# Performance work log

Measured on AMD Instinct MI355X. Metric: run time of the kernel, lower is better.

Reference implementation:

```python
import jax, jax.numpy as jnp
from jax import lax
import numpy as np

NEG_INF = -1000000000.0  # matches torch masked_fill value
POS_THRESH = -100000000.0


def setup_inputs() -> dict:
    key = jax.random.key(0)
    k1, k2, k3 = jax.random.split(key, 3)
    B, C_in, L = 1, 16, 2048
    C_out, groups, K = 16, 4, 3
    scores = jax.random.normal(k1, (B, C_in, L, L), dtype=jnp.float32)
    weight = jax.random.normal(k2, (C_out, C_in // groups, K, K), dtype=jnp.float32) * 0.1
    bias = jax.random.normal(k3, (C_out,), dtype=jnp.float32) * 0.1
    return {"scores": scores, "weight": weight, "bias": bias}


def reference(scores, weight, bias):
    B, C_in, L, _ = scores.shape
    C_out, cpg, K, _ = weight.shape
    groups = C_in // cpg
    mask = jnp.tril(jnp.ones((L, L), dtype=bool))[None, None]  # (1,1,L,L) causal

    s = scores.astype(jnp.float32)
    z = jnp.where(mask, s, NEG_INF)

    # sparsemax over last axis: sort desc, cumsum, support-size threshold
    z_sorted = -jnp.sort(-z, axis=-1)                 # descending
    cum_sum = jnp.cumsum(z_sorted, axis=-1)
    k_idx = jnp.arange(1, L + 1, dtype=z.dtype)        # (L,) broadcasts over (B,C,L,L)
    cond = (1.0 + k_idx * z_sorted > cum_sum) & (z_sorted > POS_THRESH)
    k_sp = jnp.sum(cond, axis=-1, keepdims=True)       # support size, int
    k_safe = jnp.maximum(k_sp, 1)
    cum_sum_k = jnp.take_along_axis(cum_sum, k_safe - 1, axis=-1)
    tau = (cum_sum_k - 1.0) / k_safe.astype(z.dtype)
    tau = jnp.where(k_sp == 0, jnp.inf, tau)
    probs = jnp.maximum(z - tau, 0.0)                  # (B,C_in,L,L)

    # grouped same-padded conv2d over the (L,L) score map
    out = lax.conv_general_dilated(
        probs, weight,
        window_strides=(1, 1),
        padding=[(K // 2, K // 2), (K // 2, K // 2)],
        feature_group_count=groups,
        dimension_numbers=("NCHW", "OIHW", "NCHW"),
    )
    out = out + bias[None, :, None, None]
    out = jnp.where(mask, out, 0.0)
    return out.astype(scores.dtype)
```

## Files before the change

### kernel.cpp

```cpp
#include <hip/hip_runtime.h>

#define L 2048
#define CIN 16
#define GROUPS 4
#define NEG_INF  -1000000000.0f
#define POS_THRESH -100000000.0f

__global__ __launch_bounds__(256) void tau_kernel(const float* __restrict__ scores,
                                                  float* __restrict__ tau_out) {
    const int wid  = (blockIdx.x << 2) + (threadIdx.x >> 6);
    const int lane = threadIdx.x & 63;
    const int ws   = threadIdx.x >> 6;
    const int ch   = wid >> 11;
    const int row  = wid & 2047;
    const int n    = row + 1;
    const float* zrow = scores + ((size_t)ch * L + row) * L;

    float v[32];
    float m = NEG_INF;
#pragma unroll
    for (int j = 0; j < 8; ++j) {
        int c4 = lane + (j << 6);
        int c  = c4 << 2;
        float4 z = make_float4(NEG_INF, NEG_INF, NEG_INF, NEG_INF);
        if (c < n) z = *((const float4*)zrow + c4);
        v[4*j+0] = (c + 0 < n) ? z.x : NEG_INF;
        v[4*j+1] = (c + 1 < n) ? z.y : NEG_INF;
        v[4*j+2] = (c + 2 < n) ? z.z : NEG_INF;
        v[4*j+3] = (c + 3 < n) ? z.w : NEG_INF;
        m = fmaxf(m, fmaxf(fmaxf(v[4*j+0], v[4*j+1]), fmaxf(v[4*j+2], v[4*j+3])));
    }
#pragma unroll
    for (int d = 32; d; d >>= 1) m = fmaxf(m, __shfl_xor(m, d, 64));

    const float thr = m - 1.0f;

    __shared__ float buf[4][64];
    int base = 0;
#pragma unroll
    for (int j = 0; j < 32; ++j) {
        bool p = v[j] > thr;
        unsigned long long mask = __ballot(p);
        if (mask) {
            if (p) {
                int pos = __builtin_amdgcn_mbcnt_lo((unsigned)mask, 0);
                pos = __builtin_amdgcn_mbcnt_hi((unsigned)(mask >> 32), pos);
                pos += base;
                if (pos < 64) buf[ws][pos] = v[j];
            }
            base += __popcll(mask);
        }
    }
    __syncthreads();
    const int cnt = base;

    float tau;
    if (cnt <= 64) {
        float x = (lane < cnt) ? buf[ws][lane] : NEG_INF;
#pragma unroll
        for (int k = 2; k <= 64; k <<= 1) {
#pragma unroll
            for (int j = k >> 1; j > 0; j >>= 1) {
                float p = __shfl_xor(x, j, 64);
                bool desc    = ((lane & k) == 0);
                bool earlier = ((lane & j) == 0);
                float mx = fmaxf(x, p), mn = fminf(x, p);
                x = (desc == earlier) ? mx : mn;
            }
        }
        float csum = x;
#pragma unroll
        for (int d = 1; d < 64; d <<= 1) {
            float y = __shfl_up(csum, d, 64);
            if (lane >= d) csum += y;
        }
        bool cond = (1.0f + (float)(lane + 1) * x > csum) && (x > POS_THRESH);
        unsigned long long cmask = __ballot(cond);
        int k = (int)__popcll(cmask);
        float ck = __shfl(csum, k - 1, 64);
        tau = (ck - 1.0f) / (float)k;
    } else {
        tau = thr;
        int k_prev = -1;
        for (int it = 0; it < 64; ++it) {
            float S = 0.0f, Kf = 0.0f;
#pragma unroll
            for (int j = 0; j < 32; ++j)
                if (v[j] > tau) { S += v[j]; Kf += 1.0f; }
#pragma unroll
            for (int d = 32; d; d >>= 1) {
                S  += __shfl_xor(S,  d, 64);
                Kf += __shfl_xor(Kf, d, 64);
            }
            int K = (int)Kf;
            if (K == k_prev) break;
            tau = (S - 1.0f) / Kf;
            k_prev = K;
        }
    }
    if (lane == 0) tau_out[ch * L + row] = tau;
}

#define TR 16
#define TC 64
#define HR 18
#define PST 68

struct W6 { float l, m0, m1, m2, m3, r; };

__device__ __forceinline__ float rfl(float x) {
    return __builtin_bit_cast(float,
        __builtin_amdgcn_readfirstlane(__builtin_bit_cast(int, x)));
}

__global__ __launch_bounds__(256, 4) void conv_kernel(const float* __restrict__ scores,
                                                      const float* __restrict__ tau,
                                                      const float* __restrict__ weight,
                                                      const float* __restrict__ bias,
                                                      float* __restrict__ out) {
    const int c0 = blockIdx.x * TC;
    const int r0 = blockIdx.y * TR;
    const int g  = blockIdx.z;
    const int t  = threadIdx.x;

    if (c0 > r0 + TR - 1) {
        const float4 z4 = make_float4(0.f, 0.f, 0.f, 0.f);
#pragma unroll
        for (int jj = 0; jj < 4; ++jj) {
            int idx = t + (jj << 8);
            int c4  = idx & 15;
            int r   = (idx >> 4) & 15;
            int o   = idx >> 8;
            float4* p = (float4*)(out + (((size_t)((g << 2) + o) * L + (r0 + r)) * L + c0)) + c4;
            *p = z4;
        }
        return;
    }

    __shared__ __align__(16) float P[4][HR][PST];

    const bool interior = (c0 >= 1) && (c0 + TC + 1 <= r0) && (r0 + TR <= L - 1);

    const float* sbase = scores + (size_t)(g << 2) * L * L;
    const float* tbase = tau + (g << 2) * L;

    float4 zr[5];
    float  tvr[5];

    if (interior) {
#pragma unroll
        for (int jj = 0; jj < 5; ++jj) {
            int idx = t + (jj << 8);
            if (idx < 1152) {
                int hr = idx >> 6, ic = (idx >> 4) & 3, c4 = idx & 15;
                int r  = r0 - 1 + hr;
                zr[jj]  = *((const float4*)(sbase + (size_t)ic * L * L + (size_t)r * L + c0) + c4);
                tvr[jj] = tbase[ic * L + r];
            }
        }
        float hv = 0.f;
        int hic = 0, hhr = 0, hside = 0;
        if (t < 144) {
            hside = t & 1;
            int j = t >> 1;
            hic = j / HR; hhr = j - hic * HR;
            int r = r0 - 1 + hhr;
            int c = hside ? (c0 + TC) : (c0 - 1);
            hv = fmaxf(sbase[(size_t)hic * L * L + (size_t)r * L + c] - tbase[hic * L + r], 0.f);
        }
#pragma unroll
        for (int jj = 0; jj < 5; ++jj) {
            int idx = t + (jj << 8);
            if (idx < 1152) {
                int hr = idx >> 6, ic = (idx >> 4) & 3, c4 = idx & 15;
                float tv = tvr[jj];
                float4 z = zr[jj];
                float4 val;
                val.x = fmaxf(z.x - tv, 0.f);
                val.y = fmaxf(z.y - tv, 0.f);
                val.z = fmaxf(z.z - tv, 0.f);
                val.w = fmaxf(z.w - tv, 0.f);
                *((float4*)&P[ic][hr][c4 << 2]) = val;
            }
        }
        if (t < 144) P[hic][hhr][hside ? TC : 67] = hv;
    } else {
#pragma unroll
        for (int jj = 0; jj < 5; ++jj) {
            int idx = t + (jj << 8);
            zr[jj] = make_float4(0.f, 0.f, 0.f, 0.f);
            tvr[jj] = 0.f;
            if (idx < 1152) {
                int hr = idx >> 6, ic = (idx >> 4) & 3, c4 = idx & 15;
                int r  = r0 - 1 + hr;
                int cb = c0 + (c4 << 2);
                if (r >= 0 && r < L && cb <= r) {
                    zr[jj]  = *((const float4*)(sbase + (size_t)ic * L * L + (size_t)r * L) + (cb >> 2));
                    tvr[jj] = tbase[ic * L + r];
                }
            }
        }
        float hv = 0.f;
        int hic = 0, hhr = 0, hside = 0;
        if (t < 144) {
            hside = t & 1;
            int j = t >> 1;
            hic = j / HR; hhr = j - hic * HR;
            int r = r0 - 1 + hhr;
            int c = hside ? (c0 + TC) : (c0 - 1);
            if (r >= 0 && r < L && c >= 0 && c <= r)
                hv = fmaxf(sbase[(size_t)hic * L * L + (size_t)r * L + c] - tbase[hic * L + r], 0.f);
        }
#pragma unroll
        for (int jj = 0; jj < 5; ++jj) {
            int idx = t + (jj << 8);
            if (idx < 1152) {
                int hr = idx >> 6, ic = (idx >> 4) & 3, c4 = idx & 15;
                int r  = r0 - 1 + hr;
                int cb = c0 + (c4 << 2);
                float tv = tvr[jj];
                float4 z = zr[jj];
                float4 val = make_float4(0.f, 0.f, 0.f, 0.f);
                if (r >= 0 && r < L && cb <= r) {
                    val.x = fmaxf(z.x - tv, 0.f);
                    val.y = (cb + 1 <= r) ? fmaxf(z.y - tv, 0.f) : 0.f;
                    val.z = (cb + 2 <= r) ? fmaxf(z.z - tv, 0.f) : 0.f;
                    val.w = (cb + 3 <= r) ? fmaxf(z.w - tv, 0.f) : 0.f;
                }
                *((float4*)&P[ic][hr][c4 << 2]) = val;
            }
        }
        if (t < 144) P[hic][hhr][hside ? TC : 67] = hv;
    }
    __syncthreads();

    const int w4   = t >> 6;
    const int lane = t & 63;
    const int col4 = lane & 15;
    const int rloc = lane >> 4;
    const int ro   = (w4 << 2) + rloc;
    const int obase = g << 2;
    const int cb   = c0 + (col4 << 2);
    const int li   = col4 ? ((col4 << 2) - 2) : 66;
    const int ri   = (col4 << 2) + 4;

    auto ldwin = [&](int ic, int hr) -> W6 {
        const float* rp = &P[ic][hr][0];
        float4 M  = *(const float4*)(rp + (col4 << 2));
        float2 Lv = *(const float2*)(rp + li);
        float2 Rv = *(const float2*)(rp + ri);
        W6 q; q.l = Lv.y; q.m0 = M.x; q.m1 = M.y; q.m2 = M.z; q.m3 = M.w; q.r = Rv.x;
        return q;
    };

    float4 acc[4];
#pragma unroll
    for (int oc = 0; oc < 4; ++oc) {
        float bb = rfl(bias[obase + oc]);
        acc[oc] = make_float4(bb, bb, bb, bb);
    }

#define ROWFMA(q, wa, wb, wc, A)                                           \
    A.x = fmaf(q.l,  wa, fmaf(q.m0, wb, fmaf(q.m1, wc, A.x)));             \
    A.y = fmaf(q.m0, wa, fmaf(q.m1, wb, fmaf(q.m2, wc, A.y)));             \
    A.z = fmaf(q.m1, wa, fmaf(q.m2, wb, fmaf(q.m3, wc, A.z)));             \
    A.w = fmaf(q.m2, wa, fmaf(q.m3, wb, fmaf(q.r,  wc, A.w)));

#pragma unroll
    for (int ic = 0; ic < 4; ++ic) {
        W6 q0 = ldwin(ic, ro);
        W6 q1 = ldwin(ic, ro + 1);
        W6 q2 = ldwin(ic, ro + 2);
#pragma unroll
        for (int oc = 0; oc < 4; ++oc) {
            const float* wp = weight + (((obase + oc) << 2) + ic) * 9;
            const float w00 = rfl(wp[0]), w01 = rfl(wp[1]), w02 = rfl(wp[2]);
            const float w10 = rfl(wp[3]), w11 = rfl(wp[4]), w12 = rfl(wp[5]);
            const float w20 = rfl(wp[6]), w21 = rfl(wp[7]), w22 = rfl(wp[8]);
            ROWFMA(q0, w00, w01, w02, acc[oc])
            ROWFMA(q1, w10, w11, w12, acc[oc])
            ROWFMA(q2, w20, w21, w22, acc[oc])
        }
    }
#undef ROWFMA

    const int r_out = r0 + ro;
    if (interior) {
#pragma unroll
        for (int oc = 0; oc < 4; ++oc) {
            float* outp = out + ((size_t)(obase + oc) * L + r_out) * L + cb;
            *(float4*)outp = acc[oc];
        }
    } else {
#pragma unroll
        for (int oc = 0; oc < 4; ++oc) {
            float4 res;
            res.x = (cb     <= r_out) ? acc[oc].x : 0.f;
            res.y = (cb + 1 <= r_out) ? acc[oc].y : 0.f;
            res.z = (cb + 2 <= r_out) ? acc[oc].z : 0.f;
            res.w = (cb + 3 <= r_out) ? acc[oc].w : 0.f;
            float* outp = out + ((size_t)(obase + oc) * L + r_out) * L + cb;
            *(float4*)outp = res;
        }
    }
}

extern "C" void kernel_launch(void* const* d_in, const int* in_sizes, int n_in,
                              void* d_out, int out_size, void* d_ws, size_t ws_size,
                              hipStream_t stream) {
    const float* scores = (const float*)d_in[0];
    const float* weight = (const float*)d_in[1];
    const float* bias   = (const float*)d_in[2];
    float* out = (float*)d_out;
    float* tau = (float*)d_ws;

    tau_kernel<<<(CIN * L) / 4, 256, 0, stream>>>(scores, tau);

    dim3 gridB(L / TC, L / TR, GROUPS);
    conv_kernel<<<gridB, 256, 0, stream>>>(scores, tau, weight, bias, out);
}
```

Baseline: 486.0 us.

## Double-buffer per-input-channel probability tiles in conv kernel shared memory

Instead of loading all four input channels' sparsemax-probability tiles into shared memory before computing, the conv kernel now stages one channel at a time in a two-slot shared buffer. It prefetches the next channel into registers while computing the current one. This halves shared memory per block, which may allow more blocks per CU, and overlaps global loads with FMA work. The cost is an extra barrier per channel and a longer serial dependency chain inside each block. The edge path now fills masked lanes with tau so they evaluate to zero.

```diff
diff --git a/kernel.cpp b/kernel.cpp
--- a/kernel.cpp
+++ b/kernel.cpp
@@ -107,10 +107,84 @@
 #define PST 68
 
 struct W6 { float l, m0, m1, m2, m3, r; };
+struct Stage { float4 z0, z1; float tv0, tv1, hv; };
 
 __device__ __forceinline__ float rfl(float x) {
     return __builtin_bit_cast(float,
         __builtin_amdgcn_readfirstlane(__builtin_bit_cast(int, x)));
+}
+
+template<bool CHK>
+__device__ __forceinline__ void load_stage(Stage& s, const float* __restrict__ sb,
+                                           const float* __restrict__ tb,
+                                           int r0, int c0, int t) {
+    const int hr = t >> 4, c4 = t & 15;
+    const int r  = r0 - 1 + hr;
+    const int cb = c0 + (c4 << 2);
+    if (!CHK) {
+        s.z0  = *((const float4*)(sb + (size_t)r * L + c0) + c4);
+        s.tv0 = tb[r];
+    } else {
+        s.z0 = make_float4(0.f, 0.f, 0.f, 0.f); s.tv0 = 0.f;
+        if (r >= 0 && r < L && cb <= r) {
+            s.z0  = *((const float4*)(sb + (size_t)r * L) + (cb >> 2));
+            s.tv0 = tb[r];
+            if (cb + 1 > r) s.z0.y = s.tv0;
+            if (cb + 2 > r) s.z0.z = s.tv0;
+            if (cb + 3 > r) s.z0.w = s.tv0;
+        }
+    }
+    if (t < 32) {
+        const int r1 = r0 + 15 + (t >> 4);
+        if (!CHK) {
+            s.z1  = *((const float4*)(sb + (size_t)r1 * L + c0) + c4);
+            s.tv1 = tb[r1];
+        } else {
+            s.z1 = make_float4(0.f, 0.f, 0.f, 0.f); s.tv1 = 0.f;
+            if (r1 >= 0 && r1 < L && cb <= r1) {
+                s.z1  = *((const float4*)(sb + (size_t)r1 * L) + (cb >> 2));
+                s.tv1 = tb[r1];
+                if (cb + 1 > r1) s.z1.y = s.tv1;
+                if (cb + 2 > r1) s.z1.z = s.tv1;
+                if (cb + 3 > r1) s.z1.w = s.tv1;
+            }
+        }
+    }
+    if (t >= 64 && t < 100) {
+        const int j = t - 64, side = j & 1, hhr = j >> 1;
+        const int r2 = r0 - 1 + hhr;
+        const int c  = side ? (c0 + TC) : (c0 - 1);
+        if (!CHK) {
+            s.hv = fmaxf(sb[(size_t)r2 * L + c] - tb[r2], 0.f);
+        } else {
+            s.hv = 0.f;
+            if (r2 >= 0 && r2 < L && c >= 0 && c <= r2)
+                s.hv = fmaxf(sb[(size_t)r2 * L + c] - tb[r2], 0.f);
+        }
+    }
+}
+
+__device__ __forceinline__ void store_stage(const Stage& s, float B[HR][PST], int t) {
+    const int hr = t >> 4, c4 = t & 15;
+    float4 v;
+    v.x = fmaxf(s.z0.x - s.tv0, 0.f);
+    v.y = fmaxf(s.z0.y - s.tv0, 0.f);
+    v.z = fmaxf(s.z0.z - s.tv0, 0.f);
+    v.w = fmaxf(s.z0.w - s.tv0, 0.f);
+    *((float4*)&B[hr][c4 << 2]) = v;
+    if (t < 32) {
+        const int hr1 = 16 + (t >> 4);
+        float4 u;
+        u.x = fmaxf(s.z1.x - s.tv1, 0.f);
+        u.y = fmaxf(s.z1.y - s.tv1, 0.f);
+        u.z = fmaxf(s.z1.z - s.tv1, 0.f);
+        u.w = fmaxf(s.z1.w - s.tv1, 0.f);
+        *((float4*)&B[hr1][c4 << 2]) = u;
+    }
+    if (t >= 64 && t < 100) {
+        const int j = t - 64, side = j & 1, hhr = j >> 1;
+        B[hhr][side ? TC : 67] = s.hv;
+    }
 }
 
 __global__ __launch_bounds__(256, 4) void conv_kernel(const float* __restrict__ scores,
@@ -137,102 +211,12 @@
         return;
     }
 
-    __shared__ __align__(16) float P[4][HR][PST];
+    __shared__ __align__(16) float Pb[2][HR][PST];
 
     const bool interior = (c0 >= 1) && (c0 + TC + 1 <= r0) && (r0 + TR <= L - 1);
 
     const float* sbase = scores + (size_t)(g << 2) * L * L;
     const float* tbase = tau + (g << 2) * L;
-
-    float4 zr[5];
-    float  tvr[5];
-
-    if (interior) {
-#pragma unroll
-        for (int jj = 0; jj < 5; ++jj) {
-            int idx = t + (jj << 8);
-            if (idx < 1152) {
-                int hr = idx >> 6, ic = (idx >> 4) & 3, c4 = idx & 15;
-                int r  = r0 - 1 + hr;
-                zr[jj]  = *((const float4*)(sbase + (size_t)ic * L * L + (size_t)r * L + c0) + c4);
-                tvr[jj] = tbase[ic * L + r];
-            }
-        }
-        float hv = 0.f;
-        int hic = 0, hhr = 0, hside = 0;
-        if (t < 144) {
-            hside = t & 1;
-            int j = t >> 1;
-            hic = j / HR; hhr = j - hic * HR;
-            int r = r0 - 1 + hhr;
-            int c = hside ? (c0 + TC) : (c0 - 1);
-            hv = fmaxf(sbase[(size_t)hic * L * L + (size_t)r * L + c] - tbase[hic * L + r], 0.f);
-        }
-#pragma unroll
-        for (int jj = 0; jj < 5; ++jj) {
-            int idx = t + (jj << 8);
-            if (idx < 1152) {
-                int hr = idx >> 6, ic = (idx >> 4) & 3, c4 = idx & 15;
-                float tv = tvr[jj];
-                float4 z = zr[jj];
-                float4 val;
-                val.x = fmaxf(z.x - tv, 0.f);
-                val.y = fmaxf(z.y - tv, 0.f);
-                val.z = fmaxf(z.z - tv, 0.f);
-                val.w = fmaxf(z.w - tv, 0.f);
-                *((float4*)&P[ic][hr][c4 << 2]) = val;
-            }
-        }
-        if (t < 144) P[hic][hhr][hside ? TC : 67] = hv;
-    } else {
-#pragma unroll
-        for (int jj = 0; jj < 5; ++jj) {
-            int idx = t + (jj << 8);
-            zr[jj] = make_float4(0.f, 0.f, 0.f, 0.f);
-            tvr[jj] = 0.f;
-            if (idx < 1152) {
-                int hr = idx >> 6, ic = (idx >> 4) & 3, c4 = idx & 15;
-                int r  = r0 - 1 + hr;
-                int cb = c0 + (c4 << 2);
-                if (r >= 0 && r < L && cb <= r) {
-                    zr[jj]  = *((const float4*)(sbase + (size_t)ic * L * L + (size_t)r * L) + (cb >> 2));
-                    tvr[jj] = tbase[ic * L + r];
-                }
-            }
-        }
-        float hv = 0.f;
-        int hic = 0, hhr = 0, hside = 0;
-        if (t < 144) {
-            hside = t & 1;
-            int j = t >> 1;
-            hic = j / HR; hhr = j - hic * HR;
-            int r = r0 - 1 + hhr;
-            int c = hside ? (c0 + TC) : (c0 - 1);
-            if (r >= 0 && r < L && c >= 0 && c <= r)
-                hv = fmaxf(sbase[(size_t)hic * L * L + (size_t)r * L + c] - tbase[hic * L + r], 0.f);
-        }
-#pragma unroll
-        for (int jj = 0; jj < 5; ++jj) {
-            int idx = t + (jj << 8);
-            if (idx < 1152) {
-                int hr = idx >> 6, ic = (idx >> 4) & 3, c4 = idx & 15;
-                int r  = r0 - 1 + hr;
-                int cb = c0 + (c4 << 2);
-                float tv = tvr[jj];
-                float4 z = zr[jj];
-                float4 val = make_float4(0.f, 0.f, 0.f, 0.f);
-                if (r >= 0 && r < L && cb <= r) {
-                    val.x = fmaxf(z.x - tv, 0.f);
-                    val.y = (cb + 1 <= r) ? fmaxf(z.y - tv, 0.f) : 0.f;
-                    val.z = (cb + 2 <= r) ? fmaxf(z.z - tv, 0.f) : 0.f;
-                    val.w = (cb + 3 <= r) ? fmaxf(z.w - tv, 0.f) : 0.f;
-                }
-                *((float4*)&P[ic][hr][c4 << 2]) = val;
-            }
-        }
-        if (t < 144) P[hic][hhr][hside ? TC : 67] = hv;
-    }
-    __syncthreads();
 
     const int w4   = t >> 6;
     const int lane = t & 63;
@@ -244,8 +228,8 @@
     const int li   = col4 ? ((col4 << 2) - 2) : 66;
     const int ri   = (col4 << 2) + 4;
 
-    auto ldwin = [&](int ic, int hr) -> W6 {
-        const float* rp = &P[ic][hr][0];
+    auto ldwin = [&](const float (*B)[PST], int hr) -> W6 {
+        const float* rp = &B[hr][0];
         float4 M  = *(const float4*)(rp + (col4 << 2));
         float2 Lv = *(const float2*)(rp + li);
         float2 Rv = *(const float2*)(rp + ri);
@@ -266,22 +250,57 @@
     A.z = fmaf(q.m1, wa, fmaf(q.m2, wb, fmaf(q.m3, wc, A.z)));             \
     A.w = fmaf(q.m2, wa, fmaf(q.m3, wb, fmaf(q.r,  wc, A.w)));
 
-#pragma unroll
-    for (int ic = 0; ic < 4; ++ic) {
-        W6 q0 = ldwin(ic, ro);
-        W6 q1 = ldwin(ic, ro + 1);
-        W6 q2 = ldwin(ic, ro + 2);
-#pragma unroll
-        for (int oc = 0; oc < 4; ++oc) {
-            const float* wp = weight + (((obase + oc) << 2) + ic) * 9;
-            const float w00 = rfl(wp[0]), w01 = rfl(wp[1]), w02 = rfl(wp[2]);
-            const float w10 = rfl(wp[3]), w11 = rfl(wp[4]), w12 = rfl(wp[5]);
-            const float w20 = rfl(wp[6]), w21 = rfl(wp[7]), w22 = rfl(wp[8]);
-            ROWFMA(q0, w00, w01, w02, acc[oc])
-            ROWFMA(q1, w10, w11, w12, acc[oc])
-            ROWFMA(q2, w20, w21, w22, acc[oc])
-        }
-    }
+#define COMPUTE_IC(ic, BUF)                                                \
+    {                                                                      \
+        W6 q0 = ldwin(BUF, ro);                                            \
+        W6 q1 = ldwin(BUF, ro + 1);                                        \
+        W6 q2 = ldwin(BUF, ro + 2);                                        \
+        _Pragma("unroll")                                                  \
+        for (int oc = 0; oc < 4; ++oc) {                                   \
+            const float* wp = weight + (((obase + oc) << 2) + (ic)) * 9;   \
+            const float w00 = rfl(wp[0]), w01 = rfl(wp[1]), w02 = rfl(wp[2]); \
+            const float w10 = rfl(wp[3]), w11 = rfl(wp[4]), w12 = rfl(wp[5]); \
+            const float w20 = rfl(wp[6]), w21 = rfl(wp[7]), w22 = rfl(wp[8]); \
+            ROWFMA(q0, w00, w01, w02, acc[oc])                             \
+            ROWFMA(q1, w10, w11, w12, acc[oc])                             \
+            ROWFMA(q2, w20, w21, w22, acc[oc])                             \
+        }                                                                  \
+    }
+
+    if (interior) {
+        Stage s;
+        load_stage<false>(s, sbase, tbase, r0, c0, t);
+        store_stage(s, Pb[0], t);
+        __syncthreads();
+#pragma unroll
+        for (int ic = 0; ic < 4; ++ic) {
+            Stage ns;
+            if (ic < 3)
+                load_stage<false>(ns, sbase + (size_t)(ic + 1) * L * L,
+                                  tbase + (ic + 1) * L, r0, c0, t);
+            COMPUTE_IC(ic, Pb[ic & 1])
+            if (ic < 3)
+                store_stage(ns, Pb[(ic + 1) & 1], t);
+            __syncthreads();
+        }
+    } else {
+        Stage s;
+        load_stage<true>(s, sbase, tbase, r0, c0, t);
+        store_stage(s, Pb[0], t);
+        __syncthreads();
+#pragma unroll
+        for (int ic = 0; ic < 4; ++ic) {
+            Stage ns;
+            if (ic < 3)
+                load_stage<true>(ns, sbase + (size_t)(ic + 1) * L * L,
+                                 tbase + (ic + 1) * L, r0, c0, t);
+            COMPUTE_IC(ic, Pb[ic & 1])
+            if (ic < 3)
+                store_stage(ns, Pb[(ic + 1) & 1], t);
+            __syncthreads();
+        }
+    }
+#undef COMPUTE_IC
 #undef ROWFMA
 
     const int r_out = r0 + ro;
```

Measured after the change: 506.6 us. 4.2% more time.

## Replace LDS tile staging in conv with direct global window loads

Applied to the files above, without the earlier changes.

Removes the shared-memory halo tile and the __syncthreads in the conv kernel. Each thread now loads its 3-row by 6-column window straight from global memory, relying on L1/L2 caching for neighbour reuse, and applies the tau subtraction and relu per element. This removes LDS traffic and the barrier but adds redundant global loads (each input row is read by three output rows) plus unaligned float2 halo loads.

```diff
diff --git a/kernel.cpp b/kernel.cpp
--- a/kernel.cpp
+++ b/kernel.cpp
@@ -103,14 +103,48 @@
 
 #define TR 16
 #define TC 64
-#define HR 18
-#define PST 68
 
 struct W6 { float l, m0, m1, m2, m3, r; };
 
 __device__ __forceinline__ float rfl(float x) {
     return __builtin_bit_cast(float,
         __builtin_amdgcn_readfirstlane(__builtin_bit_cast(int, x)));
+}
+
+__device__ __forceinline__ W6 win_int(const float* __restrict__ rowp, float tv, int cb) {
+    float4 M  = *(const float4*)(rowp + cb);
+    float2 Lv = *(const float2*)(rowp + cb - 2);
+    float2 Rv = *(const float2*)(rowp + cb + 4);
+    W6 q;
+    q.l  = fmaxf(Lv.y - tv, 0.f);
+    q.m0 = fmaxf(M.x  - tv, 0.f);
+    q.m1 = fmaxf(M.y  - tv, 0.f);
+    q.m2 = fmaxf(M.z  - tv, 0.f);
+    q.m3 = fmaxf(M.w  - tv, 0.f);
+    q.r  = fmaxf(Rv.x - tv, 0.f);
+    return q;
+}
+
+__device__ __forceinline__ W6 win_chk(const float* __restrict__ sb,
+                                      const float* __restrict__ tb,
+                                      int r, int cb) {
+    W6 q; q.l = q.m0 = q.m1 = q.m2 = q.m3 = q.r = 0.f;
+    if (r >= 0 && r < L) {
+        const float* rowp = sb + (size_t)r * L;
+        float tv = tb[r];
+        int lc = (cb >= 2) ? (cb - 2) : 0;
+        int rc = (cb + 4 <= L - 2) ? (cb + 4) : (L - 2);
+        float4 M  = *(const float4*)(rowp + cb);
+        float2 Lv = *(const float2*)(rowp + lc);
+        float2 Rv = *(const float2*)(rowp + rc);
+        q.l  = (cb >= 1 && cb - 1 <= r) ? fmaxf(Lv.y - tv, 0.f) : 0.f;
+        q.m0 = (cb     <= r) ? fmaxf(M.x  - tv, 0.f) : 0.f;
+        q.m1 = (cb + 1 <= r) ? fmaxf(M.y  - tv, 0.f) : 0.f;
+        q.m2 = (cb + 2 <= r) ? fmaxf(M.z  - tv, 0.f) : 0.f;
+        q.m3 = (cb + 3 <= r) ? fmaxf(M.w  - tv, 0.f) : 0.f;
+        q.r  = (cb + 4 <= r) ? fmaxf(Rv.x - tv, 0.f) : 0.f;
+    }
+    return q;
 }
 
 __global__ __launch_bounds__(256, 4) void conv_kernel(const float* __restrict__ scores,
@@ -137,121 +171,19 @@
         return;
     }
 
-    __shared__ __align__(16) float P[4][HR][PST];
-
     const bool interior = (c0 >= 1) && (c0 + TC + 1 <= r0) && (r0 + TR <= L - 1);
 
     const float* sbase = scores + (size_t)(g << 2) * L * L;
     const float* tbase = tau + (g << 2) * L;
-
-    float4 zr[5];
-    float  tvr[5];
-
-    if (interior) {
-#pragma unroll
-        for (int jj = 0; jj < 5; ++jj) {
-            int idx = t + (jj << 8);
-            if (idx < 1152) {
-                int hr = idx >> 6, ic = (idx >> 4) & 3, c4 = idx & 15;
-                int r  = r0 - 1 + hr;
-                zr[jj]  = *((const float4*)(sbase + (size_t)ic * L * L + (size_t)r * L + c0) + c4);
-                tvr[jj] = tbase[ic * L + r];
-            }
-        }
-        float hv = 0.f;
-        int hic = 0, hhr = 0, hside = 0;
-        if (t < 144) {
-            hside = t & 1;
-            int j = t >> 1;
-            hic = j / HR; hhr = j - hic * HR;
-            int r = r0 - 1 + hhr;
-            int c = hside ? (c0 + TC) : (c0 - 1);
-            hv = fmaxf(sbase[(size_t)hic * L * L + (size_t)r * L + c] - tbase[hic * L + r], 0.f);
-        }
-#pragma unroll
-        for (int jj = 0; jj < 5; ++jj) {
-            int idx = t + (jj << 8);
-            if (idx < 1152) {
-                int hr = idx >> 6, ic = (idx >> 4) & 3, c4 = idx & 15;
-                float tv = tvr[jj];
-                float4 z = zr[jj];
-                float4 val;
-                val.x = fmaxf(z.x - tv, 0.f);
-                val.y = fmaxf(z.y - tv, 0.f);
-                val.z = fmaxf(z.z - tv, 0.f);
-                val.w = fmaxf(z.w - tv, 0.f);
-                *((float4*)&P[ic][hr][c4 << 2]) = val;
-            }
-        }
-        if (t < 144) P[hic][hhr][hside ? TC : 67] = hv;
-    } else {
-#pragma unroll
-        for (int jj = 0; jj < 5; ++jj) {
-            int idx = t + (jj << 8);
-            zr[jj] = make_float4(0.f, 0.f, 0.f, 0.f);
-            tvr[jj] = 0.f;
-            if (idx < 1152) {
-                int hr = idx >> 6, ic = (idx >> 4) & 3, c4 = idx & 15;
-                int r  = r0 - 1 + hr;
-                int cb = c0 + (c4 << 2);
-                if (r >= 0 && r < L && cb <= r) {
-                    zr[jj]  = *((const float4*)(sbase + (size_t)ic * L * L + (size_t)r * L) + (cb >> 2));
-                    tvr[jj] = tbase[ic * L + r];
-                }
-            }
-        }
-        float hv = 0.f;
-        int hic = 0, hhr = 0, hside = 0;
-        if (t < 144) {
-            hside = t & 1;
-            int j = t >> 1;
-            hic = j / HR; hhr = j - hic * HR;
-            int r = r0 - 1 + hhr;
-            int c = hside ? (c0 + TC) : (c0 - 1);
-            if (r >= 0 && r < L && c >= 0 && c <= r)
-                hv = fmaxf(sbase[(size_t)hic * L * L + (size_t)r * L + c] - tbase[hic * L + r], 0.f);
-        }
-#pragma unroll
-        for (int jj = 0; jj < 5; ++jj) {
-            int idx = t + (jj << 8);
-            if (idx < 1152) {
-                int hr = idx >> 6, ic = (idx >> 4) & 3, c4 = idx & 15;
-                int r  = r0 - 1 + hr;
-                int cb = c0 + (c4 << 2);
-                float tv = tvr[jj];
-                float4 z = zr[jj];
-                float4 val = make_float4(0.f, 0.f, 0.f, 0.f);
-                if (r >= 0 && r < L && cb <= r) {
-                    val.x = fmaxf(z.x - tv, 0.f);
-                    val.y = (cb + 1 <= r) ? fmaxf(z.y - tv, 0.f) : 0.f;
-                    val.z = (cb + 2 <= r) ? fmaxf(z.z - tv, 0.f) : 0.f;
-                    val.w = (cb + 3 <= r) ? fmaxf(z.w - tv, 0.f) : 0.f;
-                }
-                *((float4*)&P[ic][hr][c4 << 2]) = val;
-            }
-        }
-        if (t < 144) P[hic][hhr][hside ? TC : 67] = hv;
-    }
-    __syncthreads();
 
     const int w4   = t >> 6;
     const int lane = t & 63;
     const int col4 = lane & 15;
     const int rloc = lane >> 4;
     const int ro   = (w4 << 2) + rloc;
+    const int r_out = r0 + ro;
     const int obase = g << 2;
     const int cb   = c0 + (col4 << 2);
-    const int li   = col4 ? ((col4 << 2) - 2) : 66;
-    const int ri   = (col4 << 2) + 4;
-
-    auto ldwin = [&](int ic, int hr) -> W6 {
-        const float* rp = &P[ic][hr][0];
-        float4 M  = *(const float4*)(rp + (col4 << 2));
-        float2 Lv = *(const float2*)(rp + li);
-        float2 Rv = *(const float2*)(rp + ri);
-        W6 q; q.l = Lv.y; q.m0 = M.x; q.m1 = M.y; q.m2 = M.z; q.m3 = M.w; q.r = Rv.x;
-        return q;
-    };
 
     float4 acc[4];
 #pragma unroll
@@ -266,25 +198,43 @@
     A.z = fmaf(q.m1, wa, fmaf(q.m2, wb, fmaf(q.m3, wc, A.z)));             \
     A.w = fmaf(q.m2, wa, fmaf(q.m3, wb, fmaf(q.r,  wc, A.w)));
 
-#pragma unroll
-    for (int ic = 0; ic < 4; ++ic) {
-        W6 q0 = ldwin(ic, ro);
-        W6 q1 = ldwin(ic, ro + 1);
-        W6 q2 = ldwin(ic, ro + 2);
-#pragma unroll
-        for (int oc = 0; oc < 4; ++oc) {
-            const float* wp = weight + (((obase + oc) << 2) + ic) * 9;
-            const float w00 = rfl(wp[0]), w01 = rfl(wp[1]), w02 = rfl(wp[2]);
-            const float w10 = rfl(wp[3]), w11 = rfl(wp[4]), w12 = rfl(wp[5]);
-            const float w20 = rfl(wp[6]), w21 = rfl(wp[7]), w22 = rfl(wp[8]);
-            ROWFMA(q0, w00, w01, w02, acc[oc])
-            ROWFMA(q1, w10, w11, w12, acc[oc])
-            ROWFMA(q2, w20, w21, w22, acc[oc])
-        }
-    }
+#define OCLOOP(ic, Q0, Q1, Q2)                                             \
+    _Pragma("unroll")                                                      \
+    for (int oc = 0; oc < 4; ++oc) {                                       \
+        const float* wp = weight + (((obase + oc) << 2) + (ic)) * 9;       \
+        const float w00 = rfl(wp[0]), w01 = rfl(wp[1]), w02 = rfl(wp[2]);  \
+        const float w10 = rfl(wp[3]), w11 = rfl(wp[4]), w12 = rfl(wp[5]);  \
+        const float w20 = rfl(wp[6]), w21 = rfl(wp[7]), w22 = rfl(wp[8]);  \
+        ROWFMA(Q0, w00, w01, w02, acc[oc])                                 \
+        ROWFMA(Q1, w10, w11, w12, acc[oc])                                 \
+        ROWFMA(Q2, w20, w21, w22, acc[oc])                                 \
+    }
+
+    if (interior) {
+#pragma unroll
+        for (int ic = 0; ic < 4; ++ic) {
+            const float* sb = sbase + (size_t)ic * L * L;
+            const float* tb = tbase + ic * L;
+            const float* rp = sb + (size_t)(r_out - 1) * L;
+            W6 q0 = win_int(rp,           tb[r_out - 1], cb);
+            W6 q1 = win_int(rp + L,       tb[r_out],     cb);
+            W6 q2 = win_int(rp + 2 * L,   tb[r_out + 1], cb);
+            OCLOOP(ic, q0, q1, q2)
+        }
+    } else {
+#pragma unroll
+        for (int ic = 0; ic < 4; ++ic) {
+            const float* sb = sbase + (size_t)ic * L * L;
+            const float* tb = tbase + ic * L;
+            W6 q0 = win_chk(sb, tb, r_out - 1, cb);
+            W6 q1 = win_chk(sb, tb, r_out,     cb);
+            W6 q2 = win_chk(sb, tb, r_out + 1, cb);
+            OCLOOP(ic, q0, q1, q2)
+        }
+    }
+#undef OCLOOP
 #undef ROWFMA
 
-    const int r_out = r0 + ro;
     if (interior) {
 #pragma unroll
         for (int oc = 0; oc < 4; ++oc) {
```

New measurement: 580.7 us. 1.19x slower.
